# Performance work log

Measured on AMD Instinct MI355X. Metric: run time of the kernel, lower is better.

Reference implementation:

```python
import jax, jax.numpy as jnp
import numpy as np

B, N, C, H, MC, LIE, KD = 2, 2048, 256, 8, 256, 3, 16
DH = C // H

def swish(x):
    return x * jax.nn.sigmoid(x)

def layernorm(x, g, b):
    m = jnp.mean(x, axis=-1, keepdims=True)
    v = jnp.var(x, axis=-1, keepdims=True)
    return (x - m) * jax.lax.rsqrt(v + 1e-5) * g + b

def setup_inputs():
    ks = jax.random.split(jax.random.key(0), 12)
    p = lambda i, shape, s: jax.random.normal(ks[i], shape, jnp.float32) * s
    return dict(
        pairwise_g=jax.random.normal(ks[0], (B, N, N, LIE), jnp.float32),
        x=jax.random.normal(ks[1], (B, N, C), jnp.float32),
        mask=jnp.ones((B, N), dtype=bool),
        ln1_g=jnp.ones((C,), jnp.float32), ln1_b=jnp.zeros((C,), jnp.float32),
        ln2_g=jnp.ones((C,), jnp.float32), ln2_b=jnp.zeros((C,), jnp.float32),
        wn_w1=p(2, (LIE, KD), 0.3), wn_b1=jnp.zeros((KD,), jnp.float32),
        wn_w2=p(3, (KD, KD), 0.3), wn_b2=jnp.zeros((KD,), jnp.float32),
        wn_w3=p(4, (KD, H), 0.3), wn_b3=jnp.zeros((H,), jnp.float32),
        wq=p(5, (C, C), 0.05), bq=jnp.zeros((C,), jnp.float32),
        wk=p(6, (C, C), 0.05), bk=jnp.zeros((C,), jnp.float32),
        in_w=p(7, (C, C), 0.05), in_b=jnp.zeros((C,), jnp.float32),
        out_w=p(8, (C, C), 0.05), out_b=jnp.zeros((C,), jnp.float32),
        mlp_w1=p(9, (C, C), 0.05), mlp_b1=jnp.zeros((C,), jnp.float32),
        mlp_w2=p(10, (C, C), 0.05), mlp_b2=jnp.zeros((C,), jnp.float32),
    )

def _ema(pairwise_g, x, mask, wn_w1, wn_b1, wn_w2, wn_b2, wn_w3, wn_b3,
         wq, bq, wk, bk, in_w, in_b, out_w, out_b):
    b, n, c = x.shape
    # neighbourhood extraction: topk smallest T(3) group distances (mc_samples=MC, fill=1.0)
    dists = jnp.linalg.norm(pairwise_g, axis=-1)                      # (b,n,n)
    dists = jnp.where(mask[:, None, :], dists, jnp.float32(1e8))
    _, idx = jax.lax.top_k(-dists, MC)                                # (b,n,k)
    nbhd_g = jnp.take_along_axis(pairwise_g, idx[..., None], axis=2)  # (b,n,k,LIE)
    nbhd_mask = jnp.take_along_axis(jnp.broadcast_to(mask[:, None, :], (b, n, n)), idx, axis=2)
    # location kernel: MultiheadWeightNet MLP on pairwise group elements -> per-head scalar
    hloc = swish(nbhd_g @ wn_w1 + wn_b1)
    hloc = swish(hloc @ wn_w2 + wn_b2)
    loc = hloc @ wn_w3 + wn_b3                                        # (b,n,k,H)
    # feature kernel: multihead dot product over gathered neighbour keys
    q = (x @ wq + bq).reshape(b, n, H, DH)
    kf = (x @ wk + bk).reshape(b, n, H, DH)
    k_nbhd = jax.vmap(lambda kfb, ib: kfb[ib])(kf, idx)               # (b,n,k,H,DH)
    scores = jnp.einsum('bnhd,bnkhd->bnkh', q, k_nbhd) / jnp.sqrt(jnp.float32(DH))
    pre = jnp.where(nbhd_mask[..., None], loc + scores, jnp.float32(-1e38))
    attn = jax.nn.softmax(pre, axis=2)                                # (b,n,k,H)
    # values; scatter attention into dense (b,n,n,H) exactly as the torch code, then aggregate
    v = (x @ in_w + in_b).reshape(b, n, H, DH)
    BS = jnp.arange(b)[:, None, None]
    NNS = jnp.arange(n)[None, :, None]
    aw = jnp.zeros((b, n, n, H), attn.dtype).at[BS, NNS, idx].set(attn)
    out = jnp.einsum('bnmh,bmhd->bnhd', aw, v).reshape(b, n, c)
    return out @ out_w + out_b

def reference(pairwise_g, x, mask, ln1_g, ln1_b, ln2_g, ln2_b,
              wn_w1, wn_b1, wn_w2, wn_b2, wn_w3, wn_b3,
              wq, bq, wk, bk, in_w, in_b, out_w, out_b,
              mlp_w1, mlp_b1, mlp_w2, mlp_b2):
    # EquivariantTransformerBlock with block_norm='layer_pre'
    x = x + _ema(pairwise_g, layernorm(x, ln1_g, ln1_b), mask,
                 wn_w1, wn_b1, wn_w2, wn_b2, wn_w3, wn_b3,
                 wq, bq, wk, bk, in_w, in_b, out_w, out_b)
    h = layernorm(x, ln2_g, ln2_b)
    x = x + (swish(h @ mlp_w1 + mlp_b1) @ mlp_w2 + mlp_b2)
    return x
```

## Files before the change

kernel.cpp:

```cpp
#include <hip/hip_runtime.h>
#include <hip/hip_bf16.h>

#define Bb 2
#define Nn 2048
#define Cc 256
#define Hh 8
#define MCk 256
#define RT (Bb * Nn)

typedef __hip_bfloat16 bf16;
typedef _Float16 f16;
typedef __fp16 h2v __attribute__((ext_vector_type(2)));
typedef __fp16 h8 __attribute__((ext_vector_type(8)));
typedef float f32x4 __attribute__((ext_vector_type(4)));
typedef float v2f __attribute__((ext_vector_type(2)));

__device__ __forceinline__ float bl(unsigned u) { return __uint_as_float(u << 16); }
__device__ __forceinline__ float bh(unsigned u) { return __uint_as_float(u & 0xFFFF0000u); }
__device__ __forceinline__ h2v bc16(unsigned u) { return __builtin_bit_cast(h2v, u); }
__device__ __forceinline__ unsigned bcu(h2v v) { return __builtin_bit_cast(unsigned, v); }

__device__ __forceinline__ float dot2(h2v a, h2v b, float c) {
  return __builtin_amdgcn_fdot2(a, b, c, false);
}
__device__ __forceinline__ f32x4 mfma16(h8 a, h8 b, f32x4 c) {
  return __builtin_amdgcn_mfma_f32_16x16x32_f16(a, b, c, 0, 0, 0);
}
__device__ __forceinline__ float swish_f(float z) {
  return z * __builtin_amdgcn_rcpf(1.f + __expf(-z));
}

__global__ __launch_bounds__(256) void prep_ln(
    const float* __restrict__ w0, const float* __restrict__ w1,
    const float* __restrict__ w2, const float* __restrict__ w3,
    const float* __restrict__ w4, const float* __restrict__ w5,
    f16* __restrict__ wtout,
    const float* __restrict__ x, const float* __restrict__ g,
    const float* __restrict__ b, f16* __restrict__ lnout)
{
  if (blockIdx.x < 384) {
    __shared__ float tile[32][33];
    int wb = blockIdx.x / 64, tid = blockIdx.x % 64;
    const float* ws_[6] = {w0, w1, w2, w3, w4, w5};
    const float* W = ws_[wb];
    f16* o = wtout + (size_t)wb * 65536;
    int tn0 = (tid & 7) * 32, tk0 = (tid >> 3) * 32;
    int tl = threadIdx.x & 31, tg = threadIdx.x >> 5;
#pragma unroll
    for (int r = 0; r < 4; r++) {
      int k = tk0 + tg * 4 + r;
      tile[tg * 4 + r][tl] = W[(size_t)k * 256 + tn0 + tl];
    }
    __syncthreads();
#pragma unroll
    for (int r = 0; r < 4; r++) {
      int n = tn0 + tg * 4 + r;
      o[(size_t)n * 256 + tk0 + tl] = (f16)tile[tl][tg * 4 + r];
    }
  } else {
    int wave = threadIdx.x >> 6, lane = threadIdx.x & 63;
    int row = (blockIdx.x - 384) * 4 + wave;
    const float4 v = reinterpret_cast<const float4*>(x + (size_t)row * Cc)[lane];
    float s  = v.x + v.y + v.z + v.w;
    float s2 = v.x * v.x + v.y * v.y + v.z * v.z + v.w * v.w;
#pragma unroll
    for (int m = 1; m < 64; m <<= 1) {
      s  += __shfl_xor(s, m);
      s2 += __shfl_xor(s2, m);
    }
    float mean = s * (1.0f / Cc);
    float var  = s2 * (1.0f / Cc) - mean * mean;
    float rs   = rsqrtf(var + 1e-5f);
    const float4 gg = reinterpret_cast<const float4*>(g)[lane];
    const float4 bb = reinterpret_cast<const float4*>(b)[lane];
    float ox = (v.x - mean) * rs * gg.x + bb.x;
    float oy = (v.y - mean) * rs * gg.y + bb.y;
    float oz = (v.z - mean) * rs * gg.z + bb.z;
    float ow = (v.w - mean) * rs * gg.w + bb.w;
    uint2 st;
    st.x = bcu(__builtin_amdgcn_cvt_pkrtz(ox, oy));
    st.y = bcu(__builtin_amdgcn_cvt_pkrtz(oz, ow));
    *(uint2*)(lnout + (size_t)row * Cc + lane * 4) = st;
  }
}

__global__ __launch_bounds__(256) void gemm_qkv_mfma(
    const f16* __restrict__ A,
    const f16* __restrict__ WTq, const float* __restrict__ Bq,
    const f16* __restrict__ WTk, const float* __restrict__ Bk,
    const f16* __restrict__ WTv, const float* __restrict__ Bv,
    f16* __restrict__ outq, f16* __restrict__ outk, bf16* __restrict__ outv)
{
  int wid = threadIdx.x >> 6, lane = threadIdx.x & 63;
  int m0 = (blockIdx.x * 4 + wid) * 16;
  int n0 = blockIdx.y * 32;
  int lm = lane & 15, lk = lane >> 4;
  const h8* Ab = (const h8*)(A + (size_t)(m0 + lm) * 256) + lk;
  const h8* Q0 = (const h8*)(WTq + (size_t)(n0 + lm) * 256) + lk;
  const h8* Q1 = (const h8*)(WTq + (size_t)(n0 + 16 + lm) * 256) + lk;
  const h8* K0 = (const h8*)(WTk + (size_t)(n0 + lm) * 256) + lk;
  const h8* K1 = (const h8*)(WTk + (size_t)(n0 + 16 + lm) * 256) + lk;
  const h8* V0 = (const h8*)(WTv + (size_t)(n0 + lm) * 256) + lk;
  const h8* V1 = (const h8*)(WTv + (size_t)(n0 + 16 + lm) * 256) + lk;
  f32x4 aq0 = {0.f,0.f,0.f,0.f}, aq1 = {0.f,0.f,0.f,0.f};
  f32x4 ak0 = {0.f,0.f,0.f,0.f}, ak1 = {0.f,0.f,0.f,0.f};
  f32x4 av0 = {0.f,0.f,0.f,0.f}, av1 = {0.f,0.f,0.f,0.f};
#pragma unroll
  for (int ks = 0; ks < 8; ks++) {
    h8 a = Ab[ks * 4];
    aq0 = mfma16(a, Q0[ks * 4], aq0);
    aq1 = mfma16(a, Q1[ks * 4], aq1);
    ak0 = mfma16(a, K0[ks * 4], ak0);
    ak1 = mfma16(a, K1[ks * 4], ak1);
    av0 = mfma16(a, V0[ks * 4], av0);
    av1 = mfma16(a, V1[ks * 4], av1);
  }
  const float qs = 0.17677669529663687f;
  float bq0 = Bq[n0 + lm], bq1 = Bq[n0 + 16 + lm];
  float bk0 = Bk[n0 + lm], bk1 = Bk[n0 + 16 + lm];
  float bv0 = Bv[n0 + lm], bv1 = Bv[n0 + 16 + lm];
#pragma unroll
  for (int i = 0; i < 4; i++) {
    size_t row = m0 + lk * 4 + i;
    outq[row * 256 + n0 + lm]      = (f16)((aq0[i] + bq0) * qs);
    outq[row * 256 + n0 + 16 + lm] = (f16)((aq1[i] + bq1) * qs);
    outk[row * 256 + n0 + lm]      = (f16)(ak0[i] + bk0);
    outk[row * 256 + n0 + 16 + lm] = (f16)(ak1[i] + bk1);
    outv[row * 256 + n0 + lm]      = __float2bfloat16(av0[i] + bv0);
    outv[row * 256 + n0 + 16 + lm] = __float2bfloat16(av1[i] + bv1);
  }
}

__global__ __launch_bounds__(256) void select_kernel(
    const float* __restrict__ pg, int* __restrict__ idxout)
{
  __shared__ int idl[4][256];
  int wave = threadIdx.x >> 6, lane = threadIdx.x & 63;
  int row = blockIdx.x * 4 + wave;
  const float* base = pg + (size_t)row * Nn * 3;
  unsigned u[32];
#pragma unroll
  for (int jj = 0; jj < 32; jj++) {
    int col = jj * 64 + lane;
    float g0 = base[col * 3 + 0];
    float g1 = base[col * 3 + 1];
    float g2 = base[col * 3 + 2];
    u[jj] = __float_as_uint(sqrtf(g0 * g0 + g1 * g1 + g2 * g2));
  }
  unsigned T = 0;
  for (int bit = 30; bit >= 0; bit--) {
    unsigned cand = T | (1u << bit);
    int c = 0;
#pragma unroll
    for (int jj = 0; jj < 32; jj++) c += (u[jj] < cand) ? 1 : 0;
#pragma unroll
    for (int m = 1; m < 64; m <<= 1) c += __shfl_xor(c, m);
    if (c <= MCk - 1) T = cand;
  }
  int cl = 0;
#pragma unroll
  for (int jj = 0; jj < 32; jj++) cl += (u[jj] < T) ? 1 : 0;
#pragma unroll
  for (int m = 1; m < 64; m <<= 1) cl += __shfl_xor(cl, m);
  int need = MCk - cl;
  unsigned long long lmask = (1ull << lane) - 1ull;
  int slot = 0;
  for (int jj = 0; jj < 32; jj++) {
    bool eq = (u[jj] == T);
    unsigned long long em = __ballot(eq);
    int ebelow = __popcll(em & lmask);
    bool sel = (u[jj] < T) || (eq && ebelow < need);
    unsigned long long smsk = __ballot(sel);
    if (sel) idl[wave][slot + __popcll(smsk & lmask)] = jj * 64 + lane;
    slot += __popcll(smsk);
    need -= __popcll(em);
    if (need < 0) need = 0;
  }
#pragma unroll
  for (int s = 0; s < 4; s++)
    idxout[(size_t)row * MCk + s * 64 + lane] = idl[wave][s * 64 + lane];
}

__global__ __launch_bounds__(256) void loc_mlp(
    const float* __restrict__ pg, const int* __restrict__ idxb,
    uint4* __restrict__ locout,
    const float* __restrict__ w1, const float* __restrict__ b1,
    const float* __restrict__ w2, const float* __restrict__ b2,
    const float* __restrict__ w3, const float* __restrict__ b3)
{
  __shared__ float wnl[64];
  __shared__ h2v   w2p[128];
  __shared__ float bn2[16];
  __shared__ h2v   w3p[64];
  __shared__ float bn3[8];
  int t = threadIdx.x;
  int row = blockIdx.x;
  for (int i = t; i < 280; i += 256) {
    if (i < 48) {
      wnl[i] = w1[i];
    } else if (i < 64) {
      wnl[i] = b1[i - 48];
    } else if (i < 192) {
      int j = i - 64, i2 = j >> 4, o = j & 15;
      w2p[j] = __builtin_amdgcn_cvt_pkrtz(w2[(2 * i2) * 16 + o], w2[(2 * i2 + 1) * 16 + o]);
    } else if (i < 208) {
      bn2[i - 192] = b2[i - 192];
    } else if (i < 272) {
      int j = i - 208, i2 = j >> 3, o = j & 7;
      w3p[j] = __builtin_amdgcn_cvt_pkrtz(w3[(2 * i2) * 8 + o], w3[(2 * i2 + 1) * 8 + o]);
    } else {
      bn3[i - 272] = b3[i - 272];
    }
  }
  int m = idxb[(size_t)row * 256 + t];
  const float* gsp = pg + ((size_t)row * Nn + m) * 3;
  float g0 = gsp[0], g1 = gsp[1], g2 = gsp[2];
  __syncthreads();
  float h1[16];
#pragma unroll
  for (int o = 0; o < 16; o++) {
    float z = wnl[48 + o] + g0 * wnl[o] + g1 * wnl[16 + o] + g2 * wnl[32 + o];
    h1[o] = swish_f(z);
  }
  h2v hp1[8];
#pragma unroll
  for (int i = 0; i < 8; i++) hp1[i] = __builtin_amdgcn_cvt_pkrtz(h1[2 * i], h1[2 * i + 1]);
  float hh[16];
#pragma unroll
  for (int o = 0; o < 16; o++) {
    float z = bn2[o];
#pragma unroll
    for (int i2 = 0; i2 < 8; i2++) z = dot2(hp1[i2], w2p[i2 * 16 + o], z);
    hh[o] = swish_f(z);
  }
  h2v hp2[8];
#pragma unroll
  for (int i = 0; i < 8; i++) hp2[i] = __builtin_amdgcn_cvt_pkrtz(hh[2 * i], hh[2 * i + 1]);
  float loc[8];
#pragma unroll
  for (int o = 0; o < 8; o++) {
    float z = bn3[o];
#pragma unroll
    for (int i2 = 0; i2 < 8; i2++) z = dot2(hp2[i2], w3p[i2 * 8 + o], z);
    loc[o] = z;
  }
  uint4 lv;
  lv.x = bcu(__builtin_amdgcn_cvt_pkrtz(loc[0], loc[1]));
  lv.y = bcu(__builtin_amdgcn_cvt_pkrtz(loc[2], loc[3]));
  lv.z = bcu(__builtin_amdgcn_cvt_pkrtz(loc[4], loc[5]));
  lv.w = bcu(__builtin_amdgcn_cvt_pkrtz(loc[6], loc[7]));
  locout[(size_t)row * 256 + t] = lv;
}

__global__ __launch_bounds__(256, 4) void attn_kernel(
    const f16* __restrict__ qh, const f16* __restrict__ kh,
    const bf16* __restrict__ vv, const int* __restrict__ idxb,
    const uint4* __restrict__ loc16, f16* __restrict__ out)
{
  __shared__ int   offs[256];
  __shared__ float ps[256 * 9];
  __shared__ float agg[4 * 256];
  __shared__ float redmx[4][8];
  __shared__ float redsm[4][8];
  int t = threadIdx.x;
  int row = blockIdx.x;
  int bidx = row >> 11;
  int g = t >> 5, c = t & 31;

  int m = idxb[(size_t)row * 256 + t];
  offs[t] = (bidx * Nn + m) * 512;
  const uint4 qu = *(const uint4*)((const char*)qh + (size_t)row * 512 + (size_t)c * 16);
  h2v q0 = bc16(qu.x), q1 = bc16(qu.y), q2 = bc16(qu.z), q3 = bc16(qu.w);
  const uint4 lv = loc16[(size_t)row * 256 + t];
  __syncthreads();

  int offr[32];
#pragma unroll
  for (int kk = 0; kk < 32; kk++) offr[kk] = offs[kk * 8 + g];

  const char* kbase = (const char*)kh + (size_t)c * 16;
#pragma unroll
  for (int kk = 0; kk < 32; kk += 4) {
    const uint4 k0 = *(const uint4*)(kbase + offr[kk + 0]);
    const uint4 k1 = *(const uint4*)(kbase + offr[kk + 1]);
    const uint4 k2 = *(const uint4*)(kbase + offr[kk + 2]);
    const uint4 k3 = *(const uint4*)(kbase + offr[kk + 3]);
    float p0 = dot2(bc16(k0.x), q0, 0.f);
    float p1 = dot2(bc16(k1.x), q0, 0.f);
    float p2 = dot2(bc16(k2.x), q0, 0.f);
    float p3 = dot2(bc16(k3.x), q0, 0.f);
    p0 = dot2(bc16(k0.y), q1, p0); p1 = dot2(bc16(k1.y), q1, p1);
    p2 = dot2(bc16(k2.y), q1, p2); p3 = dot2(bc16(k3.y), q1, p3);
    p0 = dot2(bc16(k0.z), q2, p0); p1 = dot2(bc16(k1.z), q2, p1);
    p2 = dot2(bc16(k2.z), q2, p2); p3 = dot2(bc16(k3.z), q2, p3);
    p0 = dot2(bc16(k0.w), q3, p0); p1 = dot2(bc16(k1.w), q3, p1);
    p2 = dot2(bc16(k2.w), q3, p2); p3 = dot2(bc16(k3.w), q3, p3);
    p0 += __shfl_xor(p0, 1); p1 += __shfl_xor(p1, 1);
    p2 += __shfl_xor(p2, 1); p3 += __shfl_xor(p3, 1);
    p0 += __shfl_xor(p0, 2); p1 += __shfl_xor(p1, 2);
    p2 += __shfl_xor(p2, 2); p3 += __shfl_xor(p3, 2);
    if ((c & 3) == 0) {
      int hh_ = c >> 2;
      ps[((kk + 0) * 8 + g) * 9 + hh_] = p0;
      ps[((kk + 1) * 8 + g) * 9 + hh_] = p1;
      ps[((kk + 2) * 8 + g) * 9 + hh_] = p2;
      ps[((kk + 3) * 8 + g) * 9 + hh_] = p3;
    }
  }
  __syncthreads();

  h2v l01 = bc16(lv.x), l23 = bc16(lv.y), l45 = bc16(lv.z), l67 = bc16(lv.w);
  float pre[8];
  pre[0] = ps[t * 9 + 0] + (float)l01.x;
  pre[1] = ps[t * 9 + 1] + (float)l01.y;
  pre[2] = ps[t * 9 + 2] + (float)l23.x;
  pre[3] = ps[t * 9 + 3] + (float)l23.y;
  pre[4] = ps[t * 9 + 4] + (float)l45.x;
  pre[5] = ps[t * 9 + 5] + (float)l45.y;
  pre[6] = ps[t * 9 + 6] + (float)l67.x;
  pre[7] = ps[t * 9 + 7] + (float)l67.y;
  float mx[8];
#pragma unroll
  for (int h = 0; h < 8; h++) mx[h] = pre[h];
#pragma unroll
  for (int mm = 1; mm < 64; mm <<= 1) {
#pragma unroll
    for (int h = 0; h < 8; h++) mx[h] = fmaxf(mx[h], __shfl_xor(mx[h], mm));
  }
  int wv = t >> 6, ln = t & 63;
  if (ln == 0) {
#pragma unroll
    for (int h = 0; h < 8; h++) redmx[wv][h] = mx[h];
  }
  __syncthreads();
#pragma unroll
  for (int h = 0; h < 8; h++)
    mx[h] = fmaxf(fmaxf(redmx[0][h], redmx[1][h]), fmaxf(redmx[2][h], redmx[3][h]));
  float e[8], sm[8];
#pragma unroll
  for (int h = 0; h < 8; h++) { e[h] = __expf(pre[h] - mx[h]); sm[h] = e[h]; }
#pragma unroll
  for (int mm = 1; mm < 64; mm <<= 1) {
#pragma unroll
    for (int h = 0; h < 8; h++) sm[h] += __shfl_xor(sm[h], mm);
  }
  if (ln == 0) {
#pragma unroll
    for (int h = 0; h < 8; h++) redsm[wv][h] = sm[h];
  }
  __syncthreads();
#pragma unroll
  for (int h = 0; h < 8; h++) {
    float ssum = redsm[0][h] + redsm[1][h] + redsm[2][h] + redsm[3][h];
    ps[t * 9 + h] = e[h] * __builtin_amdgcn_rcpf(ssum);
  }
  __syncthreads();

  v2f a01 = {0.f, 0.f}, a23 = {0.f, 0.f}, a45 = {0.f, 0.f}, a67 = {0.f, 0.f};
  const char* vbase = (const char*)vv + (size_t)c * 16;
  int hh_ = c >> 2;
#pragma unroll
  for (int kk = 0; kk < 32; kk += 4) {
    const uint4 v0 = *(const uint4*)(vbase + offr[kk + 0]);
    const uint4 v1 = *(const uint4*)(vbase + offr[kk + 1]);
    const uint4 v2 = *(const uint4*)(vbase + offr[kk + 2]);
    const uint4 v3 = *(const uint4*)(vbase + offr[kk + 3]);
    float aw0 = ps[((kk + 0) * 8 + g) * 9 + hh_];
    float aw1 = ps[((kk + 1) * 8 + g) * 9 + hh_];
    float aw2 = ps[((kk + 2) * 8 + g) * 9 + hh_];
    float aw3 = ps[((kk + 3) * 8 + g) * 9 + hh_];
    v2f w0 = {aw0, aw0}, w1 = {aw1, aw1}, w2 = {aw2, aw2}, w3 = {aw3, aw3};
    v2f t0, t1, t2, t3;
    t0 = (v2f){bl(v0.x), bh(v0.x)}; a01 = __builtin_elementwise_fma(w0, t0, a01);
    t1 = (v2f){bl(v0.y), bh(v0.y)}; a23 = __builtin_elementwise_fma(w0, t1, a23);
    t2 = (v2f){bl(v0.z), bh(v0.z)}; a45 = __builtin_elementwise_fma(w0, t2, a45);
    t3 = (v2f){bl(v0.w), bh(v0.w)}; a67 = __builtin_elementwise_fma(w0, t3, a67);
    t0 = (v2f){bl(v1.x), bh(v1.x)}; a01 = __builtin_elementwise_fma(w1, t0, a01);
    t1 = (v2f){bl(v1.y), bh(v1.y)}; a23 = __builtin_elementwise_fma(w1, t1, a23);
    t2 = (v2f){bl(v1.z), bh(v1.z)}; a45 = __builtin_elementwise_fma(w1, t2, a45);
    t3 = (v2f){bl(v1.w), bh(v1.w)}; a67 = __builtin_elementwise_fma(w1, t3, a67);
    t0 = (v2f){bl(v2.x), bh(v2.x)}; a01 = __builtin_elementwise_fma(w2, t0, a01);
    t1 = (v2f){bl(v2.y), bh(v2.y)}; a23 = __builtin_elementwise_fma(w2, t1, a23);
    t2 = (v2f){bl(v2.z), bh(v2.z)}; a45 = __builtin_elementwise_fma(w2, t2, a45);
    t3 = (v2f){bl(v2.w), bh(v2.w)}; a67 = __builtin_elementwise_fma(w2, t3, a67);
    t0 = (v2f){bl(v3.x), bh(v3.x)}; a01 = __builtin_elementwise_fma(w3, t0, a01);
    t1 = (v2f){bl(v3.y), bh(v3.y)}; a23 = __builtin_elementwise_fma(w3, t1, a23);
    t2 = (v2f){bl(v3.z), bh(v3.z)}; a45 = __builtin_elementwise_fma(w3, t2, a45);
    t3 = (v2f){bl(v3.w), bh(v3.w)}; a67 = __builtin_elementwise_fma(w3, t3, a67);
  }
  float acc[8] = {a01.x, a01.y, a23.x, a23.y, a45.x, a45.y, a67.x, a67.y};
#pragma unroll
  for (int i = 0; i < 8; i++) acc[i] += __shfl_xor(acc[i], 32);
  if ((t & 32) == 0) {
#pragma unroll
    for (int i = 0; i < 8; i++) agg[wv * 256 + c * 8 + i] = acc[i];
  }
  __syncthreads();
  float o = agg[t] + agg[256 + t] + agg[512 + t] + agg[768 + t];
  out[(size_t)row * 256 + t] = (f16)o;
}

__global__ __launch_bounds__(512) void gemm_out_ln(
    const f16* __restrict__ A, const f16* __restrict__ WT,
    const float* __restrict__ bias, const float* __restrict__ xres,
    const float* __restrict__ g, const float* __restrict__ b,
    float* __restrict__ x1, f16* __restrict__ hout)
{
  __shared__ float sred[8][16][2];
  int wid = threadIdx.x >> 6, lane = threadIdx.x & 63;
  int lm = lane & 15, lk = lane >> 4;
  int m0 = blockIdx.x * 16;
  const h8* Ab = (const h8*)(A + (size_t)(m0 + lm) * 256) + lk;
  const h8* Bp0 = (const h8*)(WT + (size_t)(wid * 32 + lm) * 256) + lk;
  const h8* Bp1 = (const h8*)(WT + (size_t)(wid * 32 + 16 + lm) * 256) + lk;
  f32x4 ac0 = {0,0,0,0}, ac1 = {0,0,0,0};
#pragma unroll
  for (int ks = 0; ks < 8; ks++) {
    h8 a = Ab[ks * 4];
    ac0 = mfma16(a, Bp0[ks * 4], ac0);
    ac1 = mfma16(a, Bp1[ks * 4], ac1);
  }
  int c0 = wid * 32 + lm, c1 = wid * 32 + 16 + lm;
  float b0 = bias[c0], b1 = bias[c1];
  float s[4], s2[4];
#pragma unroll
  for (int i = 0; i < 4; i++) {
    size_t row = m0 + lk * 4 + i;
    float y0 = ac0[i] + b0 + xres[row * 256 + c0];
    float y1 = ac1[i] + b1 + xres[row * 256 + c1];
    ac0[i] = y0; ac1[i] = y1;
    x1[row * 256 + c0] = y0;
    x1[row * 256 + c1] = y1;
    s[i] = y0 + y1; s2[i] = y0 * y0 + y1 * y1;
  }
#pragma unroll
  for (int mm = 1; mm < 16; mm <<= 1) {
#pragma unroll
    for (int i = 0; i < 4; i++) {
      s[i]  += __shfl_xor(s[i], mm);
      s2[i] += __shfl_xor(s2[i], mm);
    }
  }
  if (lm == 0) {
#pragma unroll
    for (int i = 0; i < 4; i++) {
      sred[wid][lk * 4 + i][0] = s[i];
      sred[wid][lk * 4 + i][1] = s2[i];
    }
  }
  __syncthreads();
  float g0 = g[c0], g1 = g[c1], bb0 = b[c0], bb1 = b[c1];
#pragma unroll
  for (int i = 0; i < 4; i++) {
    int r = lk * 4 + i;
    float ts = 0.f, ts2 = 0.f;
#pragma unroll
    for (int w = 0; w < 8; w++) { ts += sred[w][r][0]; ts2 += sred[w][r][1]; }
    float mean = ts * (1.f / 256.f);
    float var  = ts2 * (1.f / 256.f) - mean * mean;
    float rs   = rsqrtf(var + 1e-5f);
    size_t row = m0 + r;
    hout[row * 256 + c0] = (f16)((ac0[i] - mean) * rs * g0 + bb0);
    hout[row * 256 + c1] = (f16)((ac1[i] - mean) * rs * g1 + bb1);
  }
}

__global__ __launch_bounds__(512) void mlp_fused(
    const f16* __restrict__ A, const f16* __restrict__ WT1,
    const float* __restrict__ b1, const f16* __restrict__ WT2,
    const float* __restrict__ b2, const float* __restrict__ x1,
    float* __restrict__ outp)
{
  __shared__ f16 hl[16 * 272];
  int wid = threadIdx.x >> 6, lane = threadIdx.x & 63;
  int lm = lane & 15, lk = lane >> 4;
  int m0 = blockIdx.x * 16;
  const h8* Ab = (const h8*)(A + (size_t)(m0 + lm) * 256) + lk;
  const h8* B10 = (const h8*)(WT1 + (size_t)(wid * 32 + lm) * 256) + lk;
  const h8* B11 = (const h8*)(WT1 + (size_t)(wid * 32 + 16 + lm) * 256) + lk;
  const h8* B20 = (const h8*)(WT2 + (size_t)(wid * 32 + lm) * 256) + lk;
  const h8* B21 = (const h8*)(WT2 + (size_t)(wid * 32 + 16 + lm) * 256) + lk;
  f32x4 ac0 = {0,0,0,0}, ac1 = {0,0,0,0};
#pragma unroll
  for (int ks = 0; ks < 8; ks++) {
    h8 a = Ab[ks * 4];
    ac0 = mfma16(a, B10[ks * 4], ac0);
    ac1 = mfma16(a, B11[ks * 4], ac1);
  }
  int c0 = wid * 32 + lm, c1 = wid * 32 + 16 + lm;
  float bb0 = b1[c0], bb1 = b1[c1];
#pragma unroll
  for (int i = 0; i < 4; i++) {
    float y0 = ac0[i] + bb0;
    float y1 = ac1[i] + bb1;
    hl[(lk * 4 + i) * 272 + c0] = (f16)swish_f(y0);
    hl[(lk * 4 + i) * 272 + c1] = (f16)swish_f(y1);
  }
  __syncthreads();
  f32x4 o0 = {0,0,0,0}, o1 = {0,0,0,0};
#pragma unroll
  for (int ks = 0; ks < 8; ks++) {
    h8 a2 = *(const h8*)&hl[lm * 272 + ks * 32 + lk * 8];
    o0 = mfma16(a2, B20[ks * 4], o0);
    o1 = mfma16(a2, B21[ks * 4], o1);
  }
  float d0 = b2[c0], d1 = b2[c1];
#pragma unroll
  for (int i = 0; i < 4; i++) {
    size_t row = m0 + lk * 4 + i;
    outp[row * 256 + c0] = o0[i] + d0 + x1[row * 256 + c0];
    outp[row * 256 + c1] = o1[i] + d1 + x1[row * 256 + c1];
  }
}

extern "C" void kernel_launch(void* const* d_in, const int* in_sizes, int n_in,
                              void* d_out, int out_size, void* d_ws, size_t ws_size,
                              hipStream_t stream)
{
  (void)in_sizes; (void)n_in; (void)out_size; (void)ws_size;
  const float* pg   = (const float*)d_in[0];
  const float* x    = (const float*)d_in[1];
  const float* ln1g = (const float*)d_in[3];
  const float* ln1b = (const float*)d_in[4];
  const float* ln2g = (const float*)d_in[5];
  const float* ln2b = (const float*)d_in[6];
  const float* wnw1 = (const float*)d_in[7];
  const float* wnb1 = (const float*)d_in[8];
  const float* wnw2 = (const float*)d_in[9];
  const float* wnb2 = (const float*)d_in[10];
  const float* wnw3 = (const float*)d_in[11];
  const float* wnb3 = (const float*)d_in[12];
  const float* wq   = (const float*)d_in[13];
  const float* bq   = (const float*)d_in[14];
  const float* wk   = (const float*)d_in[15];
  const float* bk   = (const float*)d_in[16];
  const float* inw  = (const float*)d_in[17];
  const float* inb  = (const float*)d_in[18];
  const float* outw = (const float*)d_in[19];
  const float* outbv= (const float*)d_in[20];
  const float* m1w  = (const float*)d_in[21];
  const float* m1b  = (const float*)d_in[22];
  const float* m2w  = (const float*)d_in[23];
  const float* m2b  = (const float*)d_in[24];

  const size_t RC = (size_t)RT * 256;
  f16*   WTall = (f16*)d_ws;
  f16*   WTq = WTall + 0 * 65536;
  f16*   WTk = WTall + 1 * 65536;
  f16*   WTv = WTall + 2 * 65536;
  f16*   WTo = WTall + 3 * 65536;
  f16*   WTm1= WTall + 4 * 65536;
  f16*   WTm2= WTall + 5 * 65536;
  f16*   ln1h = WTall + 6 * 65536;
  f16*   qh  = ln1h + RC;
  f16*   kh  = qh + RC;
  bf16*  vvb = (bf16*)(kh + RC);
  int*   idxb= (int*)(vvb + RC);
  f16*   emah= (f16*)(idxb + RC);
  void*  R1  = (void*)(emah + RC);
  uint4* loc16 = (uint4*)R1;
  float* x1    = (float*)R1;
  f16*   ln2h  = ln1h;

  dim3 blk(256);
  prep_ln<<<dim3(384 + RT / 4), blk, 0, stream>>>(wq, wk, inw, outw, m1w, m2w, WTall,
                                                  x, ln1g, ln1b, ln1h);
  select_kernel<<<dim3(RT / 4), blk, 0, stream>>>(pg, idxb);
  loc_mlp<<<dim3(RT), blk, 0, stream>>>(pg, idxb, loc16,
                                        wnw1, wnb1, wnw2, wnb2, wnw3, wnb3);
  gemm_qkv_mfma<<<dim3(RT / 64, 8), blk, 0, stream>>>(ln1h, WTq, bq, WTk, bk, WTv, inb,
                                                      qh, kh, vvb);
  attn_kernel<<<dim3(RT), blk, 0, stream>>>(qh, kh, vvb, idxb, loc16, emah);
  gemm_out_ln<<<dim3(RT / 16), dim3(512), 0, stream>>>(emah, WTo, outbv, x, ln2g, ln2b,
                                                       x1, ln2h);
  mlp_fused<<<dim3(RT / 16), dim3(512), 0, stream>>>(ln2h, WTm1, m1b, WTm2, m2b, x1,
                                                     (float*)d_out);
}
```

Measured before the change: 158.4 us.

## Fuse prep/select and locmlp/qkv launches, block-wide select, fp16 packed value accumulation

Merges the weight transpose, layernorm and top-k selection into one launch, and the location MLP and QKV GEMM into a second, cutting the launch count from seven to five. Selection moves from one row per wave to one row per 256-thread block, with cross-wave counts combined through shared memory and block barriers, which spreads the per-row radix search across more threads. V is stored as fp16 and the attention value aggregation uses packed fp16 FMAs instead of unpacking bf16 to fp32. The fp16 accumulation over 256 neighbours lowers precision, and the selection now needs about 40 block barriers per row.

```diff
diff --git a/kernel.cpp b/kernel.cpp
--- a/kernel.cpp
+++ b/kernel.cpp
@@ -13,10 +13,7 @@
 typedef __fp16 h2v __attribute__((ext_vector_type(2)));
 typedef __fp16 h8 __attribute__((ext_vector_type(8)));
 typedef float f32x4 __attribute__((ext_vector_type(4)));
-typedef float v2f __attribute__((ext_vector_type(2)));
-
-__device__ __forceinline__ float bl(unsigned u) { return __uint_as_float(u << 16); }
-__device__ __forceinline__ float bh(unsigned u) { return __uint_as_float(u & 0xFFFF0000u); }
+
 __device__ __forceinline__ h2v bc16(unsigned u) { return __builtin_bit_cast(h2v, u); }
 __device__ __forceinline__ unsigned bcu(h2v v) { return __builtin_bit_cast(unsigned, v); }
 
@@ -30,22 +27,28 @@
   return z * __builtin_amdgcn_rcpf(1.f + __expf(-z));
 }
 
-__global__ __launch_bounds__(256) void prep_ln(
+__global__ __launch_bounds__(256) void k1_prep_ln_select(
     const float* __restrict__ w0, const float* __restrict__ w1,
     const float* __restrict__ w2, const float* __restrict__ w3,
     const float* __restrict__ w4, const float* __restrict__ w5,
     f16* __restrict__ wtout,
     const float* __restrict__ x, const float* __restrict__ g,
-    const float* __restrict__ b, f16* __restrict__ lnout)
+    const float* __restrict__ b, f16* __restrict__ lnout,
+    const float* __restrict__ pg, int* __restrict__ idxout)
 {
-  if (blockIdx.x < 384) {
-    __shared__ float tile[32][33];
-    int wb = blockIdx.x / 64, tid = blockIdx.x % 64;
+  __shared__ float tile[32][33];
+  __shared__ int rc[31][4];
+  __shared__ int rcl[4];
+  __shared__ int em[8][4][2];
+  int bx = blockIdx.x;
+  int t = threadIdx.x;
+  if (bx < 384) {
+    int wb = bx / 64, tid = bx % 64;
     const float* ws_[6] = {w0, w1, w2, w3, w4, w5};
     const float* W = ws_[wb];
     f16* o = wtout + (size_t)wb * 65536;
     int tn0 = (tid & 7) * 32, tk0 = (tid >> 3) * 32;
-    int tl = threadIdx.x & 31, tg = threadIdx.x >> 5;
+    int tl = t & 31, tg = t >> 5;
 #pragma unroll
     for (int r = 0; r < 4; r++) {
       int k = tk0 + tg * 4 + r;
@@ -57,9 +60,9 @@
       int n = tn0 + tg * 4 + r;
       o[(size_t)n * 256 + tk0 + tl] = (f16)tile[tl][tg * 4 + r];
     }
-  } else {
-    int wave = threadIdx.x >> 6, lane = threadIdx.x & 63;
-    int row = (blockIdx.x - 384) * 4 + wave;
+  } else if (bx < 1408) {
+    int wave = t >> 6, lane = t & 63;
+    int row = (bx - 384) * 4 + wave;
     const float4 v = reinterpret_cast<const float4*>(x + (size_t)row * Cc)[lane];
     float s  = v.x + v.y + v.z + v.w;
     float s2 = v.x * v.x + v.y * v.y + v.z * v.z + v.w * v.w;
@@ -81,112 +84,80 @@
     st.x = bcu(__builtin_amdgcn_cvt_pkrtz(ox, oy));
     st.y = bcu(__builtin_amdgcn_cvt_pkrtz(oz, ow));
     *(uint2*)(lnout + (size_t)row * Cc + lane * 4) = st;
-  }
-}
-
-__global__ __launch_bounds__(256) void gemm_qkv_mfma(
+  } else {
+    int row = bx - 1408;
+    int wave = t >> 6, lane = t & 63;
+    const float* base = pg + (size_t)row * (Nn * 3);
+    unsigned u[8];
+#pragma unroll
+    for (int jj = 0; jj < 8; jj++) {
+      int col = jj * 256 + t;
+      float g0 = base[col * 3 + 0];
+      float g1 = base[col * 3 + 1];
+      float g2 = base[col * 3 + 2];
+      u[jj] = __float_as_uint(sqrtf(g0 * g0 + g1 * g1 + g2 * g2));
+    }
+    unsigned long long lmask = (1ull << lane) - 1ull;
+    unsigned T = 0;
+    for (int bit = 30; bit >= 0; bit--) {
+      unsigned cand = T | (1u << bit);
+      int c = 0;
+#pragma unroll
+      for (int jj = 0; jj < 8; jj++) c += (u[jj] < cand) ? 1 : 0;
+#pragma unroll
+      for (int m = 1; m < 64; m <<= 1) c += __shfl_xor(c, m);
+      if (lane == 0) rc[bit][wave] = c;
+      __syncthreads();
+      c = rc[bit][0] + rc[bit][1] + rc[bit][2] + rc[bit][3];
+      if (c <= MCk - 1) T = cand;
+    }
+    int cl = 0;
+#pragma unroll
+    for (int jj = 0; jj < 8; jj++) cl += (u[jj] < T) ? 1 : 0;
+#pragma unroll
+    for (int m = 1; m < 64; m <<= 1) cl += __shfl_xor(cl, m);
+    if (lane == 0) rcl[wave] = cl;
+    __syncthreads();
+    int need = MCk - (rcl[0] + rcl[1] + rcl[2] + rcl[3]);
+    int slotBase = 0, eqBase = 0;
+    for (int jj = 0; jj < 8; jj++) {
+      bool less = u[jj] < T, eq = (u[jj] == T);
+      unsigned long long bls = __ballot(less), beq = __ballot(eq);
+      if (lane == 0) {
+        em[jj][wave][0] = __popcll(bls);
+        em[jj][wave][1] = __popcll(beq);
+      }
+      __syncthreads();
+      int lessPref = 0, lessTot = 0, eqPref = 0, eqTot = 0;
+#pragma unroll
+      for (int w = 0; w < 4; w++) {
+        int lw = em[jj][w][0], ew = em[jj][w][1];
+        lessTot += lw; eqTot += ew;
+        if (w < wave) { lessPref += lw; eqPref += ew; }
+      }
+      int epb = eqPref + __popcll(beq & lmask);
+      int rem = need - eqBase; if (rem < 0) rem = 0;
+      bool sel = less || (eq && (epb < rem));
+      int takenBefore = (epb < rem) ? epb : rem;
+      int pos = slotBase + lessPref + __popcll(bls & lmask) + takenBefore;
+      if (sel) idxout[(size_t)row * MCk + pos] = jj * 256 + t;
+      slotBase += lessTot + ((eqTot < rem) ? eqTot : rem);
+      eqBase += eqTot;
+    }
+  }
+}
+
+__global__ __launch_bounds__(256) void k2_locmlp_qkv(
+    const float* __restrict__ pg, const int* __restrict__ idxb,
+    uint4* __restrict__ locout,
+    const float* __restrict__ w1, const float* __restrict__ b1,
+    const float* __restrict__ w2, const float* __restrict__ b2,
+    const float* __restrict__ w3, const float* __restrict__ b3,
     const f16* __restrict__ A,
     const f16* __restrict__ WTq, const float* __restrict__ Bq,
     const f16* __restrict__ WTk, const float* __restrict__ Bk,
     const f16* __restrict__ WTv, const float* __restrict__ Bv,
-    f16* __restrict__ outq, f16* __restrict__ outk, bf16* __restrict__ outv)
-{
-  int wid = threadIdx.x >> 6, lane = threadIdx.x & 63;
-  int m0 = (blockIdx.x * 4 + wid) * 16;
-  int n0 = blockIdx.y * 32;
-  int lm = lane & 15, lk = lane >> 4;
-  const h8* Ab = (const h8*)(A + (size_t)(m0 + lm) * 256) + lk;
-  const h8* Q0 = (const h8*)(WTq + (size_t)(n0 + lm) * 256) + lk;
-  const h8* Q1 = (const h8*)(WTq + (size_t)(n0 + 16 + lm) * 256) + lk;
-  const h8* K0 = (const h8*)(WTk + (size_t)(n0 + lm) * 256) + lk;
-  const h8* K1 = (const h8*)(WTk + (size_t)(n0 + 16 + lm) * 256) + lk;
-  const h8* V0 = (const h8*)(WTv + (size_t)(n0 + lm) * 256) + lk;
-  const h8* V1 = (const h8*)(WTv + (size_t)(n0 + 16 + lm) * 256) + lk;
-  f32x4 aq0 = {0.f,0.f,0.f,0.f}, aq1 = {0.f,0.f,0.f,0.f};
-  f32x4 ak0 = {0.f,0.f,0.f,0.f}, ak1 = {0.f,0.f,0.f,0.f};
-  f32x4 av0 = {0.f,0.f,0.f,0.f}, av1 = {0.f,0.f,0.f,0.f};
-#pragma unroll
-  for (int ks = 0; ks < 8; ks++) {
-    h8 a = Ab[ks * 4];
-    aq0 = mfma16(a, Q0[ks * 4], aq0);
-    aq1 = mfma16(a, Q1[ks * 4], aq1);
-    ak0 = mfma16(a, K0[ks * 4], ak0);
-    ak1 = mfma16(a, K1[ks * 4], ak1);
-    av0 = mfma16(a, V0[ks * 4], av0);
-    av1 = mfma16(a, V1[ks * 4], av1);
-  }
-  const float qs = 0.17677669529663687f;
-  float bq0 = Bq[n0 + lm], bq1 = Bq[n0 + 16 + lm];
-  float bk0 = Bk[n0 + lm], bk1 = Bk[n0 + 16 + lm];
-  float bv0 = Bv[n0 + lm], bv1 = Bv[n0 + 16 + lm];
-#pragma unroll
-  for (int i = 0; i < 4; i++) {
-    size_t row = m0 + lk * 4 + i;
-    outq[row * 256 + n0 + lm]      = (f16)((aq0[i] + bq0) * qs);
-    outq[row * 256 + n0 + 16 + lm] = (f16)((aq1[i] + bq1) * qs);
-    outk[row * 256 + n0 + lm]      = (f16)(ak0[i] + bk0);
-    outk[row * 256 + n0 + 16 + lm] = (f16)(ak1[i] + bk1);
-    outv[row * 256 + n0 + lm]      = __float2bfloat16(av0[i] + bv0);
-    outv[row * 256 + n0 + 16 + lm] = __float2bfloat16(av1[i] + bv1);
-  }
-}
-
-__global__ __launch_bounds__(256) void select_kernel(
-    const float* __restrict__ pg, int* __restrict__ idxout)
-{
-  __shared__ int idl[4][256];
-  int wave = threadIdx.x >> 6, lane = threadIdx.x & 63;
-  int row = blockIdx.x * 4 + wave;
-  const float* base = pg + (size_t)row * Nn * 3;
-  unsigned u[32];
-#pragma unroll
-  for (int jj = 0; jj < 32; jj++) {
-    int col = jj * 64 + lane;
-    float g0 = base[col * 3 + 0];
-    float g1 = base[col * 3 + 1];
-    float g2 = base[col * 3 + 2];
-    u[jj] = __float_as_uint(sqrtf(g0 * g0 + g1 * g1 + g2 * g2));
-  }
-  unsigned T = 0;
-  for (int bit = 30; bit >= 0; bit--) {
-    unsigned cand = T | (1u << bit);
-    int c = 0;
-#pragma unroll
-    for (int jj = 0; jj < 32; jj++) c += (u[jj] < cand) ? 1 : 0;
-#pragma unroll
-    for (int m = 1; m < 64; m <<= 1) c += __shfl_xor(c, m);
-    if (c <= MCk - 1) T = cand;
-  }
-  int cl = 0;
-#pragma unroll
-  for (int jj = 0; jj < 32; jj++) cl += (u[jj] < T) ? 1 : 0;
-#pragma unroll
-  for (int m = 1; m < 64; m <<= 1) cl += __shfl_xor(cl, m);
-  int need = MCk - cl;
-  unsigned long long lmask = (1ull << lane) - 1ull;
-  int slot = 0;
-  for (int jj = 0; jj < 32; jj++) {
-    bool eq = (u[jj] == T);
-    unsigned long long em = __ballot(eq);
-    int ebelow = __popcll(em & lmask);
-    bool sel = (u[jj] < T) || (eq && ebelow < need);
-    unsigned long long smsk = __ballot(sel);
-    if (sel) idl[wave][slot + __popcll(smsk & lmask)] = jj * 64 + lane;
-    slot += __popcll(smsk);
-    need -= __popcll(em);
-    if (need < 0) need = 0;
-  }
-#pragma unroll
-  for (int s = 0; s < 4; s++)
-    idxout[(size_t)row * MCk + s * 64 + lane] = idl[wave][s * 64 + lane];
-}
-
-__global__ __launch_bounds__(256) void loc_mlp(
-    const float* __restrict__ pg, const int* __restrict__ idxb,
-    uint4* __restrict__ locout,
-    const float* __restrict__ w1, const float* __restrict__ b1,
-    const float* __restrict__ w2, const float* __restrict__ b2,
-    const float* __restrict__ w3, const float* __restrict__ b3)
+    f16* __restrict__ outq, f16* __restrict__ outk, f16* __restrict__ outv)
 {
   __shared__ float wnl[64];
   __shared__ h2v   w2p[128];
@@ -194,67 +165,109 @@
   __shared__ h2v   w3p[64];
   __shared__ float bn3[8];
   int t = threadIdx.x;
-  int row = blockIdx.x;
-  for (int i = t; i < 280; i += 256) {
-    if (i < 48) {
-      wnl[i] = w1[i];
-    } else if (i < 64) {
-      wnl[i] = b1[i - 48];
-    } else if (i < 192) {
-      int j = i - 64, i2 = j >> 4, o = j & 15;
-      w2p[j] = __builtin_amdgcn_cvt_pkrtz(w2[(2 * i2) * 16 + o], w2[(2 * i2 + 1) * 16 + o]);
-    } else if (i < 208) {
-      bn2[i - 192] = b2[i - 192];
-    } else if (i < 272) {
-      int j = i - 208, i2 = j >> 3, o = j & 7;
-      w3p[j] = __builtin_amdgcn_cvt_pkrtz(w3[(2 * i2) * 8 + o], w3[(2 * i2 + 1) * 8 + o]);
-    } else {
-      bn3[i - 272] = b3[i - 272];
-    }
-  }
-  int m = idxb[(size_t)row * 256 + t];
-  const float* gsp = pg + ((size_t)row * Nn + m) * 3;
-  float g0 = gsp[0], g1 = gsp[1], g2 = gsp[2];
-  __syncthreads();
-  float h1[16];
-#pragma unroll
-  for (int o = 0; o < 16; o++) {
-    float z = wnl[48 + o] + g0 * wnl[o] + g1 * wnl[16 + o] + g2 * wnl[32 + o];
-    h1[o] = swish_f(z);
-  }
-  h2v hp1[8];
-#pragma unroll
-  for (int i = 0; i < 8; i++) hp1[i] = __builtin_amdgcn_cvt_pkrtz(h1[2 * i], h1[2 * i + 1]);
-  float hh[16];
-#pragma unroll
-  for (int o = 0; o < 16; o++) {
-    float z = bn2[o];
-#pragma unroll
-    for (int i2 = 0; i2 < 8; i2++) z = dot2(hp1[i2], w2p[i2 * 16 + o], z);
-    hh[o] = swish_f(z);
-  }
-  h2v hp2[8];
-#pragma unroll
-  for (int i = 0; i < 8; i++) hp2[i] = __builtin_amdgcn_cvt_pkrtz(hh[2 * i], hh[2 * i + 1]);
-  float loc[8];
-#pragma unroll
-  for (int o = 0; o < 8; o++) {
-    float z = bn3[o];
-#pragma unroll
-    for (int i2 = 0; i2 < 8; i2++) z = dot2(hp2[i2], w3p[i2 * 8 + o], z);
-    loc[o] = z;
-  }
-  uint4 lv;
-  lv.x = bcu(__builtin_amdgcn_cvt_pkrtz(loc[0], loc[1]));
-  lv.y = bcu(__builtin_amdgcn_cvt_pkrtz(loc[2], loc[3]));
-  lv.z = bcu(__builtin_amdgcn_cvt_pkrtz(loc[4], loc[5]));
-  lv.w = bcu(__builtin_amdgcn_cvt_pkrtz(loc[6], loc[7]));
-  locout[(size_t)row * 256 + t] = lv;
+  if (blockIdx.x < 4096) {
+    int row = blockIdx.x;
+    for (int i = t; i < 280; i += 256) {
+      if (i < 48) {
+        wnl[i] = w1[i];
+      } else if (i < 64) {
+        wnl[i] = b1[i - 48];
+      } else if (i < 192) {
+        int j = i - 64, i2 = j >> 4, o = j & 15;
+        w2p[j] = __builtin_amdgcn_cvt_pkrtz(w2[(2 * i2) * 16 + o], w2[(2 * i2 + 1) * 16 + o]);
+      } else if (i < 208) {
+        bn2[i - 192] = b2[i - 192];
+      } else if (i < 272) {
+        int j = i - 208, i2 = j >> 3, o = j & 7;
+        w3p[j] = __builtin_amdgcn_cvt_pkrtz(w3[(2 * i2) * 8 + o], w3[(2 * i2 + 1) * 8 + o]);
+      } else {
+        bn3[i - 272] = b3[i - 272];
+      }
+    }
+    int m = idxb[(size_t)row * 256 + t];
+    const float* gsp = pg + ((size_t)row * Nn + m) * 3;
+    float g0 = gsp[0], g1 = gsp[1], g2 = gsp[2];
+    __syncthreads();
+    float h1[16];
+#pragma unroll
+    for (int o = 0; o < 16; o++) {
+      float z = wnl[48 + o] + g0 * wnl[o] + g1 * wnl[16 + o] + g2 * wnl[32 + o];
+      h1[o] = swish_f(z);
+    }
+    h2v hp1[8];
+#pragma unroll
+    for (int i = 0; i < 8; i++) hp1[i] = __builtin_amdgcn_cvt_pkrtz(h1[2 * i], h1[2 * i + 1]);
+    float hh[16];
+#pragma unroll
+    for (int o = 0; o < 16; o++) {
+      float z = bn2[o];
+#pragma unroll
+      for (int i2 = 0; i2 < 8; i2++) z = dot2(hp1[i2], w2p[i2 * 16 + o], z);
+      hh[o] = swish_f(z);
+    }
+    h2v hp2[8];
+#pragma unroll
+    for (int i = 0; i < 8; i++) hp2[i] = __builtin_amdgcn_cvt_pkrtz(hh[2 * i], hh[2 * i + 1]);
+    float loc[8];
+#pragma unroll
+    for (int o = 0; o < 8; o++) {
+      float z = bn3[o];
+#pragma unroll
+      for (int i2 = 0; i2 < 8; i2++) z = dot2(hp2[i2], w3p[i2 * 8 + o], z);
+      loc[o] = z;
+    }
+    uint4 lv;
+    lv.x = bcu(__builtin_amdgcn_cvt_pkrtz(loc[0], loc[1]));
+    lv.y = bcu(__builtin_amdgcn_cvt_pkrtz(loc[2], loc[3]));
+    lv.z = bcu(__builtin_amdgcn_cvt_pkrtz(loc[4], loc[5]));
+    lv.w = bcu(__builtin_amdgcn_cvt_pkrtz(loc[6], loc[7]));
+    locout[(size_t)row * 256 + t] = lv;
+  } else {
+    int bxq = blockIdx.x - 4096;
+    int wid = t >> 6, lane = t & 63;
+    int m0 = ((bxq & 63) * 4 + wid) * 16;
+    int n0 = (bxq >> 6) * 32;
+    int lm = lane & 15, lk = lane >> 4;
+    const h8* Ab = (const h8*)(A + (size_t)(m0 + lm) * 256) + lk;
+    const h8* Q0 = (const h8*)(WTq + (size_t)(n0 + lm) * 256) + lk;
+    const h8* Q1 = (const h8*)(WTq + (size_t)(n0 + 16 + lm) * 256) + lk;
+    const h8* K0 = (const h8*)(WTk + (size_t)(n0 + lm) * 256) + lk;
+    const h8* K1 = (const h8*)(WTk + (size_t)(n0 + 16 + lm) * 256) + lk;
+    const h8* V0 = (const h8*)(WTv + (size_t)(n0 + lm) * 256) + lk;
+    const h8* V1 = (const h8*)(WTv + (size_t)(n0 + 16 + lm) * 256) + lk;
+    f32x4 aq0 = {0.f,0.f,0.f,0.f}, aq1 = {0.f,0.f,0.f,0.f};
+    f32x4 ak0 = {0.f,0.f,0.f,0.f}, ak1 = {0.f,0.f,0.f,0.f};
+    f32x4 av0 = {0.f,0.f,0.f,0.f}, av1 = {0.f,0.f,0.f,0.f};
+#pragma unroll
+    for (int ks = 0; ks < 8; ks++) {
+      h8 a = Ab[ks * 4];
+      aq0 = mfma16(a, Q0[ks * 4], aq0);
+      aq1 = mfma16(a, Q1[ks * 4], aq1);
+      ak0 = mfma16(a, K0[ks * 4], ak0);
+      ak1 = mfma16(a, K1[ks * 4], ak1);
+      av0 = mfma16(a, V0[ks * 4], av0);
+      av1 = mfma16(a, V1[ks * 4], av1);
+    }
+    const float qs = 0.17677669529663687f;
+    float bq0 = Bq[n0 + lm], bq1 = Bq[n0 + 16 + lm];
+    float bk0 = Bk[n0 + lm], bk1 = Bk[n0 + 16 + lm];
+    float bv0 = Bv[n0 + lm], bv1 = Bv[n0 + 16 + lm];
+#pragma unroll
+    for (int i = 0; i < 4; i++) {
+      size_t row = m0 + lk * 4 + i;
+      outq[row * 256 + n0 + lm]      = (f16)((aq0[i] + bq0) * qs);
+      outq[row * 256 + n0 + 16 + lm] = (f16)((aq1[i] + bq1) * qs);
+      outk[row * 256 + n0 + lm]      = (f16)(ak0[i] + bk0);
+      outk[row * 256 + n0 + 16 + lm] = (f16)(ak1[i] + bk1);
+      outv[row * 256 + n0 + lm]      = (f16)(av0[i] + bv0);
+      outv[row * 256 + n0 + 16 + lm] = (f16)(av1[i] + bv1);
+    }
+  }
 }
 
 __global__ __launch_bounds__(256, 4) void attn_kernel(
     const f16* __restrict__ qh, const f16* __restrict__ kh,
-    const bf16* __restrict__ vv, const int* __restrict__ idxb,
+    const f16* __restrict__ vv, const int* __restrict__ idxb,
     const uint4* __restrict__ loc16, f16* __restrict__ out)
 {
   __shared__ int   offs[256];
@@ -356,7 +369,7 @@
   }
   __syncthreads();
 
-  v2f a01 = {0.f, 0.f}, a23 = {0.f, 0.f}, a45 = {0.f, 0.f}, a67 = {0.f, 0.f};
+  h2v ac0 = {0, 0}, ac1 = {0, 0}, ac2 = {0, 0}, ac3 = {0, 0};
   const char* vbase = (const char*)vv + (size_t)c * 16;
   int hh_ = c >> 2;
 #pragma unroll
@@ -369,26 +382,21 @@
     float aw1 = ps[((kk + 1) * 8 + g) * 9 + hh_];
     float aw2 = ps[((kk + 2) * 8 + g) * 9 + hh_];
     float aw3 = ps[((kk + 3) * 8 + g) * 9 + hh_];
-    v2f w0 = {aw0, aw0}, w1 = {aw1, aw1}, w2 = {aw2, aw2}, w3 = {aw3, aw3};
-    v2f t0, t1, t2, t3;
-    t0 = (v2f){bl(v0.x), bh(v0.x)}; a01 = __builtin_elementwise_fma(w0, t0, a01);
-    t1 = (v2f){bl(v0.y), bh(v0.y)}; a23 = __builtin_elementwise_fma(w0, t1, a23);
-    t2 = (v2f){bl(v0.z), bh(v0.z)}; a45 = __builtin_elementwise_fma(w0, t2, a45);
-    t3 = (v2f){bl(v0.w), bh(v0.w)}; a67 = __builtin_elementwise_fma(w0, t3, a67);
-    t0 = (v2f){bl(v1.x), bh(v1.x)}; a01 = __builtin_elementwise_fma(w1, t0, a01);
-    t1 = (v2f){bl(v1.y), bh(v1.y)}; a23 = __builtin_elementwise_fma(w1, t1, a23);
-    t2 = (v2f){bl(v1.z), bh(v1.z)}; a45 = __builtin_elementwise_fma(w1, t2, a45);
-    t3 = (v2f){bl(v1.w), bh(v1.w)}; a67 = __builtin_elementwise_fma(w1, t3, a67);
-    t0 = (v2f){bl(v2.x), bh(v2.x)}; a01 = __builtin_elementwise_fma(w2, t0, a01);
-    t1 = (v2f){bl(v2.y), bh(v2.y)}; a23 = __builtin_elementwise_fma(w2, t1, a23);
-    t2 = (v2f){bl(v2.z), bh(v2.z)}; a45 = __builtin_elementwise_fma(w2, t2, a45);
-    t3 = (v2f){bl(v2.w), bh(v2.w)}; a67 = __builtin_elementwise_fma(w2, t3, a67);
-    t0 = (v2f){bl(v3.x), bh(v3.x)}; a01 = __builtin_elementwise_fma(w3, t0, a01);
-    t1 = (v2f){bl(v3.y), bh(v3.y)}; a23 = __builtin_elementwise_fma(w3, t1, a23);
-    t2 = (v2f){bl(v3.z), bh(v3.z)}; a45 = __builtin_elementwise_fma(w3, t2, a45);
-    t3 = (v2f){bl(v3.w), bh(v3.w)}; a67 = __builtin_elementwise_fma(w3, t3, a67);
-  }
-  float acc[8] = {a01.x, a01.y, a23.x, a23.y, a45.x, a45.y, a67.x, a67.y};
+    h2v w0 = __builtin_amdgcn_cvt_pkrtz(aw0, aw0);
+    h2v w1 = __builtin_amdgcn_cvt_pkrtz(aw1, aw1);
+    h2v w2 = __builtin_amdgcn_cvt_pkrtz(aw2, aw2);
+    h2v w3 = __builtin_amdgcn_cvt_pkrtz(aw3, aw3);
+    ac0 = bc16(v0.x) * w0 + ac0; ac1 = bc16(v0.y) * w0 + ac1;
+    ac2 = bc16(v0.z) * w0 + ac2; ac3 = bc16(v0.w) * w0 + ac3;
+    ac0 = bc16(v1.x) * w1 + ac0; ac1 = bc16(v1.y) * w1 + ac1;
+    ac2 = bc16(v1.z) * w1 + ac2; ac3 = bc16(v1.w) * w1 + ac3;
+    ac0 = bc16(v2.x) * w2 + ac0; ac1 = bc16(v2.y) * w2 + ac1;
+    ac2 = bc16(v2.z) * w2 + ac2; ac3 = bc16(v2.w) * w2 + ac3;
+    ac0 = bc16(v3.x) * w3 + ac0; ac1 = bc16(v3.y) * w3 + ac1;
+    ac2 = bc16(v3.z) * w3 + ac2; ac3 = bc16(v3.w) * w3 + ac3;
+  }
+  float acc[8] = {(float)ac0.x, (float)ac0.y, (float)ac1.x, (float)ac1.y,
+                  (float)ac2.x, (float)ac2.y, (float)ac3.x, (float)ac3.y};
 #pragma unroll
   for (int i = 0; i < 8; i++) acc[i] += __shfl_xor(acc[i], 32);
   if ((t & 32) == 0) {
@@ -554,7 +562,7 @@
   f16*   ln1h = WTall + 6 * 65536;
   f16*   qh  = ln1h + RC;
   f16*   kh  = qh + RC;
-  bf16*  vvb = (bf16*)(kh + RC);
+  f16*   vvb = kh + RC;
   int*   idxb= (int*)(vvb + RC);
   f16*   emah= (f16*)(idxb + RC);
   void*  R1  = (void*)(emah + RC);
@@ -563,13 +571,11 @@
   f16*   ln2h  = ln1h;
 
   dim3 blk(256);
-  prep_ln<<<dim3(384 + RT / 4), blk, 0, stream>>>(wq, wk, inw, outw, m1w, m2w, WTall,
-                                                  x, ln1g, ln1b, ln1h);
-  select_kernel<<<dim3(RT / 4), blk, 0, stream>>>(pg, idxb);
-  loc_mlp<<<dim3(RT), blk, 0, stream>>>(pg, idxb, loc16,
-                                        wnw1, wnb1, wnw2, wnb2, wnw3, wnb3);
-  gemm_qkv_mfma<<<dim3(RT / 64, 8), blk, 0, stream>>>(ln1h, WTq, bq, WTk, bk, WTv, inb,
-                                                      qh, kh, vvb);
+  k1_prep_ln_select<<<dim3(384 + RT / 4 + RT), blk, 0, stream>>>(
+      wq, wk, inw, outw, m1w, m2w, WTall, x, ln1g, ln1b, ln1h, pg, idxb);
+  k2_locmlp_qkv<<<dim3(RT + 512), blk, 0, stream>>>(
+      pg, idxb, loc16, wnw1, wnb1, wnw2, wnb2, wnw3, wnb3,
+      ln1h, WTq, bq, WTk, bk, WTv, inb, qh, kh, vvb);
   attn_kernel<<<dim3(RT), blk, 0, stream>>>(qh, kh, vvb, idxb, loc16, emah);
   gemm_out_ln<<<dim3(RT / 16), dim3(512), 0, stream>>>(emah, WTo, outbv, x, ln2g, ln2b,
                                                        x1, ln2h);
```

Measured after the change: 169.5 us. +7.0%, slower.
